# Kernel tuning notes

Measured on AMD Instinct MI355X. Metric: run time of the kernel, lower is better.

## Reference

```python
import jax, jax.numpy as jnp
import numpy as np
import math

NUM_SECTORS = 8
HIDDEN = 128
FEAT = 64
MAX_DIST = 10.0


def gru_last(x, Wih, Whh, bih, bhh):
    # PyTorch GRU (gate order r,z,n); x: (B,T,D) -> last hidden (B,H)
    B = x.shape[0]
    H = Whh.shape[1]
    xp = jnp.einsum('btd,gd->btg', x, Wih) + bih  # (B,T,3H)

    def step(h, xpt):
        hp = h @ Whh.T + bhh
        xr, xz, xn = jnp.split(xpt, 3, -1)
        hr, hz, hn = jnp.split(hp, 3, -1)
        r = jax.nn.sigmoid(xr + hr)
        z = jax.nn.sigmoid(xz + hz)
        n = jnp.tanh(xn + r * hn)
        h_new = (1.0 - z) * n + z * h
        return h_new, None

    h0 = jnp.zeros((B, H), x.dtype)
    hT, _ = jax.lax.scan(step, h0, jnp.swapaxes(xp, 0, 1))
    return hT


def setup_inputs() -> dict:
    key = jax.random.key(0)
    ks = iter(jax.random.split(key, 32))
    B, N, T = 2048, 64, 8
    H, Hn = HIDDEN, HIDDEN // 2
    s = 0.05

    def p(shape):
        return jax.random.normal(next(ks), shape, jnp.float32) * s

    inp = {
        'target_trajectory': jax.random.normal(next(ks), (B, T, 2), jnp.float32),
        'neighbor_trajectories': jax.random.normal(next(ks), (B, N, T, 2), jnp.float32),
        'relative_angles': jax.random.uniform(next(ks), (B, N), jnp.float32) * (2.0 * math.pi),
        'neighbor_mask': (jax.random.uniform(next(ks), (B, N)) > 0.2).astype(jnp.float32),
        # target GRU (H=128)
        'Wih_t': p((3 * H, 2)), 'Whh_t': p((3 * H, H)), 'bih_t': p((3 * H,)), 'bhh_t': p((3 * H,)),
        # neighbor GRU (H=64)
        'Wih_n': p((3 * Hn, 2)), 'Whh_n': p((3 * Hn, Hn)), 'bih_n': p((3 * Hn,)), 'bhh_n': p((3 * Hn,)),
        # sector encoder: 68 -> 128 -> 128
        'W1': p((H, 4 + Hn)), 'b1': p((H,)), 'W2': p((H, H)), 'b2': p((H,)),
        # fusion: 1152 -> 256 -> 128 -> 64
        'Wf1': p((2 * H, H + NUM_SECTORS * H)), 'bf1': p((2 * H,)),
        'Wf2': p((H, 2 * H)), 'bf2': p((H,)),
        'Wf3': p((FEAT, H)), 'bf3': p((FEAT,)),
        'ln_g': jnp.ones((FEAT,), jnp.float32), 'ln_b': jnp.zeros((FEAT,), jnp.float32),
    }
    return inp


def reference(target_trajectory, neighbor_trajectories, relative_angles, neighbor_mask,
              Wih_t, Whh_t, bih_t, bhh_t, Wih_n, Whh_n, bih_n, bhh_n,
              W1, b1, W2, b2, Wf1, bf1, Wf2, bf2, Wf3, bf3, ln_g, ln_b):
    B, N, T, D = neighbor_trajectories.shape
    S = NUM_SECTORS

    # trajectory encoders
    target_feature = gru_last(target_trajectory, Wih_t, Whh_t, bih_t, bhh_t)  # (B,128)
    nf = gru_last(neighbor_trajectories.reshape(B * N, T, D), Wih_n, Whh_n, bih_n, bhh_n)
    nf = nf.reshape(B, N, -1)  # (B,N,64)

    # geometry
    target_pos = target_trajectory[:, -1, :]                      # (B,2)
    npos = neighbor_trajectories[:, :, -1, :]                     # (B,N,2)
    dist = jnp.linalg.norm(npos - target_pos[:, None, :], axis=-1)  # (B,N)
    vel = neighbor_trajectories[:, :, -1, :] - neighbor_trajectories[:, :, -2, :]  # (B,N,2)

    # sector assignment (vectorized segment reduce over sectors)
    sector_size = 2.0 * math.pi / S
    sid = jnp.clip((relative_angles / sector_size).astype(jnp.int32), 0, S - 1)  # (B,N)
    valid = neighbor_mask > 0
    memb = ((sid[..., None] == jnp.arange(S)) & valid[..., None]).astype(dist.dtype)  # (B,N,S)

    count = memb.sum(1)                        # (B,S)
    nonempty = count > 0
    safe = jnp.maximum(count, 1.0)
    avg_d = jnp.where(nonempty, (dist[..., None] * memb).sum(1) / safe, 0.0)  # (B,S)
    avg_v = jnp.where(nonempty[..., None], jnp.einsum('bns,bnc->bsc', memb, vel) / safe[..., None], 0.0)

    w = jnp.exp(-dist / MAX_DIST)              # (B,N)
    wm = w[..., None] * memb                   # (B,N,S)
    wsum = wm.sum(1) + 1e-8                    # (B,S)
    wfeat = jnp.einsum('bns,bnh->bsh', wm, nf) / wsum[..., None]  # (B,S,64)

    sector_feats = jnp.concatenate([count[..., None], avg_d[..., None], avg_v, wfeat], axis=-1)  # (B,S,68)

    # sector encoder MLP (dropout off / eval)
    h = jax.nn.relu(sector_feats @ W1.T + b1)
    h = jax.nn.relu(h @ W2.T + b2)             # (B,S,128)
    enc = h.reshape(B, S * HIDDEN)

    combined = jnp.concatenate([target_feature, enc], axis=-1)  # (B,1152)
    f = jax.nn.relu(combined @ Wf1.T + bf1)
    f = jax.nn.relu(f @ Wf2.T + bf2)
    f = jax.nn.relu(f @ Wf3.T + bf3)           # (B,64)

    mu = f.mean(-1, keepdims=True)
    var = ((f - mu) ** 2).mean(-1, keepdims=True)
    return (f - mu) / jnp.sqrt(var + 1e-5) * ln_g + ln_b
```

## Files before the change

kernel.cpp:

```cpp
#include <hip/hip_runtime.h>

typedef __attribute__((ext_vector_type(8))) short short8;
typedef __attribute__((ext_vector_type(4))) float f32x4;

#define SGC (-1.44269504088896341f)
#define THC ( 2.88539008177792681f)

__device__ __forceinline__ unsigned short f2bf(float f){
  unsigned u = __float_as_uint(f);
  return (unsigned short)((u + 0x7fffu + ((u >> 16) & 1u)) >> 16);
}
__device__ __forceinline__ float bf2f(unsigned short b){
  return __uint_as_float(((unsigned)b) << 16);
}
__device__ __forceinline__ unsigned f2bf_cvt(float f){
  unsigned r;
  asm("v_cvt_pk_bf16_f32 %0, %1, %1" : "=v"(r) : "v"(f));
  return r;
}
__device__ __forceinline__ unsigned f2bf_pk(float lo, float hi){
  unsigned r;
  asm("v_cvt_pk_bf16_f32 %0, %1, %2" : "=v"(r) : "v"(lo), "v"(hi));
  return r;
}

__global__ __launch_bounds__(256) void k_prep(
    const float* __restrict__ Whh_t, const float* __restrict__ W1,
    const float* __restrict__ W2,    const float* __restrict__ Wf1,
    const float* __restrict__ Wf2,   const float* __restrict__ Wf3,
    const float* __restrict__ Whh_n,
    unsigned short* __restrict__ wgt)
{
  int i = blockIdx.x * 256 + threadIdx.x;
  if (i < 49152){
    int g = i >> 7;
    float s = (g < 256) ? SGC : THC;
    wgt[i] = f2bf(Whh_t[i] * s); return;
  }
  i -= 49152;
  if (i < 12288){ int r = i / 96, c = i % 96;
    wgt[49152 + i] = (c < 68) ? f2bf(W1[r*68 + c]) : (unsigned short)0; return; }
  i -= 12288;
  if (i < 16384){ wgt[61440 + i] = f2bf(W2[i]); return; }
  i -= 16384;
  if (i < 294912){ wgt[77824 + i] = f2bf(Wf1[i]); return; }
  i -= 294912;
  if (i < 32768){ wgt[372736 + i] = f2bf(Wf2[i]); return; }
  i -= 32768;
  if (i < 8192){ wgt[405504 + i] = f2bf(Wf3[i]); return; }
  i -= 8192;
  if (i < 12288){
    int g = i >> 6;
    float s = (g < 128) ? SGC : THC;
    wgt[413696 + i] = f2bf(Whh_n[i] * s); return;
  }
}

__global__ __launch_bounds__(256, 4) void k_gru_n(
    const float* __restrict__ ttraj, const float* __restrict__ ntraj,
    const float* __restrict__ rang,  const float* __restrict__ nmask,
    const float* __restrict__ Wih_n,
    const float* __restrict__ bih_n, const float* __restrict__ bhh_n,
    const unsigned short* __restrict__ wgt,
    const float* __restrict__ b1, const float* __restrict__ b2,
    unsigned short* __restrict__ combined)
{
  __shared__ char smem[38912];
  const int tid = threadIdx.x;
  const int w = tid >> 6, u = (tid >> 4) & 3, c = tid & 15;
  const int b = blockIdx.x;
  const unsigned short* whhN_b = wgt + 413696;

  unsigned short* whh2 = (unsigned short*)smem;
  unsigned short* wx   = whh2 + 12288;
  unsigned short* hall = (unsigned short*)(smem + 27648);
  unsigned short* hb   = hall + w * 1152;
  unsigned* xpk = (unsigned*)(smem + 36864);
  float* pool   = (float*)(smem + 36864);
  unsigned short* sfl = whh2;
  unsigned short* h1l = whh2 + 1536;

  for (int i = tid; i < 1536; i += 256){
    int nt = i >> 7, rem = i & 127;
    int hf = rem >> 6, uu = (rem >> 4) & 3, cc = rem & 15;
    *(short8*)&whh2[nt*1024 + hf*512 + (uu*16+cc)*8] =
        *(const short8*)&whhN_b[(nt*16+cc)*64 + hf*32 + uu*8];
  }
  if (tid < 192){
    int t = tid >> 4, cc = tid & 15;
    float s = (t < 8) ? SGC : THC;
    int g = (t < 4) ? (t*16 + cc) : (t < 8) ? (64 + (t-4)*16 + cc) : (128 + (t-8)*16 + cc);
    float bsum = (t < 8) ? (bih_n[g] + bhh_n[g]) : bih_n[g];
    unsigned short* p = &wx[t*128 + cc*8];
    *(short8*)p = (short8){0,0,0,0,0,0,0,0};
    p[0] = f2bf(Wih_n[g*2]   * s);
    p[1] = f2bf(Wih_n[g*2+1] * s);
    p[2] = f2bf(bsum * s);
  }
  {
    float4 v = ((const float4*)(ntraj + (size_t)b * 1024))[tid];
    int n = tid >> 2, p = (tid & 3) * 2;
    xpk[p*64 + n]       = f2bf_pk(v.x, v.y);
    xpk[(p+1)*64 + n]   = f2bf_pk(v.z, v.w);
  }
  __syncthreads();

  float bh_[4];
#pragma unroll
  for (int gt = 0; gt < 4; ++gt) bh_[gt] = bhh_n[128 + gt*16 + c] * THC;

  float hcur[4][4];
#pragma unroll
  for (int gt=0; gt<4; ++gt)
#pragma unroll
    for (int q=0; q<4; ++q) hcur[gt][q] = 0.0f;

  auto gates = [&](int gt, const f32x4& aR, const f32x4& aZ, const f32x4& aN, const f32x4& aX){
#pragma unroll
    for (int q = 0; q < 4; ++q){
      float r = __builtin_amdgcn_rcpf(1.0f + __builtin_amdgcn_exp2f(aR[q]));
      float z = __builtin_amdgcn_rcpf(1.0f + __builtin_amdgcn_exp2f(aZ[q]));
      float hn = aN[q] + bh_[gt];
      float pn = __builtin_fmaf(r, hn, aX[q]);
      float E = __builtin_amdgcn_exp2f(pn);
      float n = __builtin_fmaf(-2.0f, __builtin_amdgcn_rcpf(E + 1.0f), 1.0f);
      float hnew = __builtin_fmaf(z, hcur[gt][q] - n, n);
      hcur[gt][q] = hnew;
      hb[(u*4+q)*72 + gt*16 + c] = (unsigned short)f2bf_cvt(hnew);
    }
  };

  const int lane8 = (u*16 + c) * 8;
  const f32x4 zz = {0.f,0.f,0.f,0.f};

#pragma unroll 1
  for (int st = 0; st < 8; ++st){
    unsigned p01 = xpk[st*64 + w*16 + c];
    bool u0 = (u == 0);
    union { unsigned ui[4]; short8 s8; } a2u;
    a2u.ui[0] = u0 ? p01 : 0u;
    a2u.ui[1] = u0 ? 0x3F80u : 0u;
    a2u.ui[2] = 0u; a2u.ui[3] = 0u;
    short8 a2 = a2u.s8;

    if (st > 0){
      short8 a0 = *(short8*)&hb[c*72 + u*8];
      short8 a1 = *(short8*)&hb[c*72 + 32 + u*8];
#pragma unroll
      for (int gt = 0; gt < 4; ++gt){
        const unsigned short* pr = whh2 + gt*1024 + lane8;
        const unsigned short* pz = whh2 + (4+gt)*1024 + lane8;
        const unsigned short* pq = whh2 + (8+gt)*1024 + lane8;
        short8 bxr = *(const short8*)&wx[gt*128 + c*8];
        short8 bxz = *(const short8*)&wx[(4+gt)*128 + c*8];
        short8 bxn = *(const short8*)&wx[(8+gt)*128 + c*8];
        f32x4 aR = __builtin_amdgcn_mfma_f32_16x16x32_bf16(a0, *(const short8*)pr, zz, 0,0,0);
        aR = __builtin_amdgcn_mfma_f32_16x16x32_bf16(a1, *(const short8*)(pr+512), aR, 0,0,0);
        aR = __builtin_amdgcn_mfma_f32_16x16x32_bf16(a2, bxr, aR, 0,0,0);
        f32x4 aZ = __builtin_amdgcn_mfma_f32_16x16x32_bf16(a0, *(const short8*)pz, zz, 0,0,0);
        aZ = __builtin_amdgcn_mfma_f32_16x16x32_bf16(a1, *(const short8*)(pz+512), aZ, 0,0,0);
        aZ = __builtin_amdgcn_mfma_f32_16x16x32_bf16(a2, bxz, aZ, 0,0,0);
        f32x4 aN = __builtin_amdgcn_mfma_f32_16x16x32_bf16(a0, *(const short8*)pq, zz, 0,0,0);
        aN = __builtin_amdgcn_mfma_f32_16x16x32_bf16(a1, *(const short8*)(pq+512), aN, 0,0,0);
        f32x4 aX = __builtin_amdgcn_mfma_f32_16x16x32_bf16(a2, bxn, zz, 0,0,0);
        gates(gt, aR, aZ, aN, aX);
      }
    } else {
#pragma unroll
      for (int gt = 0; gt < 4; ++gt){
        short8 bxr = *(const short8*)&wx[gt*128 + c*8];
        short8 bxz = *(const short8*)&wx[(4+gt)*128 + c*8];
        short8 bxn = *(const short8*)&wx[(8+gt)*128 + c*8];
        f32x4 aR = __builtin_amdgcn_mfma_f32_16x16x32_bf16(a2, bxr, zz, 0,0,0);
        f32x4 aZ = __builtin_amdgcn_mfma_f32_16x16x32_bf16(a2, bxz, zz, 0,0,0);
        f32x4 aX = __builtin_amdgcn_mfma_f32_16x16x32_bf16(a2, bxn, zz, 0,0,0);
        gates(gt, aR, aZ, zz, aX);
      }
    }
  }
  __syncthreads();

  for (int i = tid; i < 1536; i += 256) sfl[i] = 0;
  if (tid < 64){
    int n = tid;
    const float* nb = ntraj + (size_t)b*1024 + n*16;
    float px = nb[14], py = nb[15];
    float vx = px - nb[12], vy = py - nb[13];
    float m   = nmask[(size_t)b*64 + n];
    float ang = rang[(size_t)b*64 + n];
    float tx = ttraj[(size_t)b*16 + 14], ty = ttraj[(size_t)b*16 + 15];
    float dx = px - tx, dy = py - ty;
    float dist = __builtin_amdgcn_sqrtf(dx*dx + dy*dy);
    int sid = (int)(ang / 0.78539816339744830962f);
    sid = sid < 0 ? 0 : (sid > 7 ? 7 : sid);
    bool valid = m > 0.0f;
    float wv = valid ? __builtin_amdgcn_exp2f(dist * -0.14426950408889634f) : 0.0f;
    pool[n]       = valid ? dist : 0.0f;
    pool[64 + n]  = valid ? vx   : 0.0f;
    pool[128 + n] = valid ? vy   : 0.0f;
    pool[192 + n] = wv;
    pool[256 + n] = valid ? (float)sid : -1.0f;
  }
  __syncthreads();
  if (tid < 8){
    int s = tid;
    float cnt=0.f, sd=0.f, sx=0.f, sy=0.f, sw=0.f;
#pragma unroll 4
    for (int n=0; n<64; ++n){
      if (pool[256+n] == (float)s){
        cnt += 1.f; sd += pool[n]; sx += pool[64+n]; sy += pool[128+n]; sw += pool[192+n];
      }
    }
    float inv = (cnt > 0.f) ? __builtin_amdgcn_rcpf(cnt) : 0.f;
    pool[320 + s] = cnt;
    pool[328 + s] = sd * inv;
    pool[336 + s] = sx * inv;
    pool[344 + s] = sy * inv;
    pool[352 + s] = __builtin_amdgcn_rcpf(sw + 1e-8f);
  }
  __syncthreads();
#pragma unroll
  for (int rep = 0; rep < 2; ++rep){
    int p = tid + rep*256;
    int s = p >> 6, h = p & 63;
    float fs = (float)s;
    float a = 0.f;
#pragma unroll 4
    for (int n = 0; n < 64; ++n){
      float wmv = (pool[256+n] == fs) ? pool[192+n] : 0.f;
      float nf  = bf2f(hall[(n>>4)*1152 + (n&15)*72 + h]);
      a += wmv * nf;
    }
    sfl[s*96 + 4 + h] = (unsigned short)f2bf_cvt(a * pool[352+s]);
  }
  if (tid < 32){
    int s = tid >> 2, cc = tid & 3;
    sfl[s*96 + cc] = (unsigned short)f2bf_cvt(pool[320 + cc*8 + s]);
  }
  __syncthreads();

  const unsigned short* w1b = wgt + 49152;
  const unsigned short* w2b = wgt + 61440;
  f32x4 accA[2];
#pragma unroll
  for (int i=0;i<2;++i) accA[i] = zz;
#pragma unroll
  for (int kc=0; kc<3; ++kc){
    short8 a = (short8){0,0,0,0,0,0,0,0};
    if (c < 8) a = *(const short8*)&sfl[c*96 + kc*32 + u*8];
#pragma unroll
    for (int i=0;i<2;++i){
      int nt = w*2 + i;
      short8 bb = *(const short8*)&w1b[(nt*16+c)*96 + kc*32 + u*8];
      accA[i] = __builtin_amdgcn_mfma_f32_16x16x32_bf16(a, bb, accA[i], 0,0,0);
    }
  }
#pragma unroll
  for (int i=0;i<2;++i){
    int nt = w*2 + i;
    float bias = b1[nt*16 + c];
#pragma unroll
    for (int q=0;q<4;++q){
      float v = accA[i][q] + bias; v = v > 0.f ? v : 0.f;
      h1l[(u*4+q)*136 + nt*16 + c] = (unsigned short)f2bf_cvt(v);
    }
  }
  __syncthreads();

  f32x4 accB[2];
#pragma unroll
  for (int i=0;i<2;++i) accB[i] = zz;
#pragma unroll
  for (int kc=0; kc<4; ++kc){
    short8 a = *(short8*)&h1l[c*136 + kc*32 + u*8];
#pragma unroll
    for (int i=0;i<2;++i){
      int nt = w*2 + i;
      short8 bb = *(const short8*)&w2b[(nt*16+c)*128 + kc*32 + u*8];
      accB[i] = __builtin_amdgcn_mfma_f32_16x16x32_bf16(a, bb, accB[i], 0,0,0);
    }
  }
#pragma unroll
  for (int i=0;i<2;++i){
    int nt = w*2 + i;
    float bias = b2[nt*16 + c];
#pragma unroll
    for (int q=0;q<4;++q){
      int row = u*4 + q;
      if (row < 8){
        float v = accB[i][q] + bias; v = v > 0.f ? v : 0.f;
        combined[(size_t)b*1152 + 128 + row*128 + nt*16 + c] = (unsigned short)f2bf_cvt(v);
      }
    }
  }
}

__global__ __launch_bounds__(256) void k_gru_t(
    const float* __restrict__ ttraj,
    const float* __restrict__ Wih_t, const float* __restrict__ bih_t, const float* __restrict__ bhh_t,
    const unsigned short* __restrict__ wgt,
    unsigned short* __restrict__ combined)
{
  __shared__ char smem[9728];
  const int tid = threadIdx.x, w = tid >> 6, u = (tid >> 4) & 3, c = tid & 15;
  unsigned short* hb0 = (unsigned short*)smem;
  unsigned short* hb1 = (unsigned short*)(smem + 4352);
  float* xs = (float*)(smem + 8704);

  xs[tid] = ttraj[(size_t)blockIdx.x*256 + tid];

  int ntg[6];
  ntg[0] = 2*w; ntg[1] = 2*w+1;
  ntg[2] = 8+2*w; ntg[3] = 9+2*w;
  ntg[4] = 16+2*w; ntg[5] = 17+2*w;

  short8 Bf[6][4];
#pragma unroll
  for (int lt2 = 0; lt2 < 6; ++lt2){
    const unsigned short* wp = wgt + (ntg[lt2]*16 + c)*128 + u*8;
#pragma unroll
    for (int kk = 0; kk < 4; ++kk)
      Bf[lt2][kk] = *(const short8*)(wp + kk*32);
  }

  float Wr0[2],Wr1[2],BR[2],Wz0[2],Wz1[2],BZ[2],Wn0[2],Wn1[2],BI[2],BH[2];
#pragma unroll
  for (int gt = 0; gt < 2; ++gt){
    int g = w*32 + gt*16 + c;
    Wr0[gt]=Wih_t[g*2]*SGC;        Wr1[gt]=Wih_t[g*2+1]*SGC;        BR[gt]=(bih_t[g]+bhh_t[g])*SGC;
    Wz0[gt]=Wih_t[(128+g)*2]*SGC;  Wz1[gt]=Wih_t[(128+g)*2+1]*SGC;  BZ[gt]=(bih_t[128+g]+bhh_t[128+g])*SGC;
    Wn0[gt]=Wih_t[(256+g)*2]*THC;  Wn1[gt]=Wih_t[(256+g)*2+1]*THC;  BI[gt]=bih_t[256+g]*THC; BH[gt]=bhh_t[256+g]*THC;
  }
  float hcur[2][4];
#pragma unroll
  for (int gt=0; gt<2; ++gt)
#pragma unroll
    for (int q=0; q<4; ++q) hcur[gt][q] = 0.0f;
  __syncthreads();

#pragma unroll 1
  for (int st = 0; st < 8; ++st){
    unsigned short* rbuf = (st & 1) ? hb0 : hb1;
    unsigned short* wbuf = (st & 1) ? hb1 : hb0;
    f32x4 acc[6];
    if (st > 0){
      short8 a0 = *(short8*)&rbuf[c*136 + u*8];
      short8 a1 = *(short8*)&rbuf[c*136 + 32 + u*8];
      short8 a2 = *(short8*)&rbuf[c*136 + 64 + u*8];
      short8 a3 = *(short8*)&rbuf[c*136 + 96 + u*8];
#pragma unroll
      for (int lt2 = 0; lt2 < 6; ++lt2){
        f32x4 t = {0.f,0.f,0.f,0.f};
        t = __builtin_amdgcn_mfma_f32_16x16x32_bf16(a0, Bf[lt2][0], t, 0,0,0);
        t = __builtin_amdgcn_mfma_f32_16x16x32_bf16(a1, Bf[lt2][1], t, 0,0,0);
        t = __builtin_amdgcn_mfma_f32_16x16x32_bf16(a2, Bf[lt2][2], t, 0,0,0);
        acc[lt2] = __builtin_amdgcn_mfma_f32_16x16x32_bf16(a3, Bf[lt2][3], t, 0,0,0);
      }
    } else {
#pragma unroll
      for (int lt2 = 0; lt2 < 6; ++lt2) acc[lt2] = (f32x4){0.f,0.f,0.f,0.f};
    }
#pragma unroll
    for (int gt = 0; gt < 2; ++gt){
#pragma unroll
      for (int q = 0; q < 4; ++q){
        int sq = u*4 + q;
        float x0 = xs[sq*16 + st*2], x1 = xs[sq*16 + st*2 + 1];
        float rp = __builtin_fmaf(Wr0[gt], x0, __builtin_fmaf(Wr1[gt], x1, acc[gt][q] + BR[gt]));
        float zp = __builtin_fmaf(Wz0[gt], x0, __builtin_fmaf(Wz1[gt], x1, acc[2+gt][q] + BZ[gt]));
        float r = __builtin_amdgcn_rcpf(1.0f + __builtin_amdgcn_exp2f(rp));
        float z = __builtin_amdgcn_rcpf(1.0f + __builtin_amdgcn_exp2f(zp));
        float hnv = acc[4+gt][q] + BH[gt];
        float pn = __builtin_fmaf(Wn0[gt], x0, __builtin_fmaf(Wn1[gt], x1, __builtin_fmaf(r, hnv, BI[gt])));
        float E = __builtin_amdgcn_exp2f(pn);
        float n = __builtin_fmaf(-2.0f, __builtin_amdgcn_rcpf(E + 1.0f), 1.0f);
        float hnew = __builtin_fmaf(z, hcur[gt][q] - n, n);
        hcur[gt][q] = hnew;
        if (st < 7){
          wbuf[sq*136 + w*32 + gt*16 + c] = (unsigned short)f2bf_cvt(hnew);
        } else {
          int row = blockIdx.x*16 + sq;
          combined[(size_t)row*1152 + w*32 + gt*16 + c] = (unsigned short)f2bf_cvt(hnew);
        }
      }
    }
    if (st < 7) __syncthreads();
  }
}

__global__ __launch_bounds__(256) void k_head(
    const unsigned short* __restrict__ combined,
    const unsigned short* __restrict__ wgt,
    const float* __restrict__ bf1, const float* __restrict__ bf2, const float* __restrict__ bf3,
    const float* __restrict__ lng, const float* __restrict__ lnb,
    float* __restrict__ out)
{
  __shared__ char smem[15104];
  const int tid = threadIdx.x, w = tid >> 6, u = (tid >> 4) & 3, c = tid & 15;
  unsigned short* f1b = (unsigned short*)smem;
  unsigned short* f2b = (unsigned short*)(smem + 8448);
  float* bf1s = (float*)(smem + 12800); float* bf2s = (float*)(smem + 13824);
  float* bf3s = (float*)(smem + 14336);
  float* lngs = (float*)(smem + 14592); float* lnbs = (float*)(smem + 14848);
  const unsigned short* wf1b = wgt + 77824;
  const unsigned short* wf2b = wgt + 372736;
  const unsigned short* wf3b = wgt + 405504;
  bf1s[tid] = bf1[tid];
  if (tid < 128) bf2s[tid] = bf2[tid];
  if (tid < 64){ bf3s[tid] = bf3[tid]; lngs[tid] = lng[tid]; lnbs[tid] = lnb[tid]; }
  __syncthreads();
  const int rowb = blockIdx.x * 16;

  f32x4 acc[4];
#pragma unroll
  for (int i=0; i<4; ++i) acc[i] = (f32x4){0.f,0.f,0.f,0.f};
#pragma unroll 4
  for (int kc=0; kc<36; ++kc){
    short8 a = *(const short8*)&combined[(size_t)(rowb + c)*1152 + kc*32 + u*8];
#pragma unroll
    for (int i=0; i<4; ++i){
      int nt = w*4 + i;
      short8 bb = *(const short8*)&wf1b[(size_t)(nt*16+c)*1152 + kc*32 + u*8];
      acc[i] = __builtin_amdgcn_mfma_f32_16x16x32_bf16(a, bb, acc[i], 0,0,0);
    }
  }
#pragma unroll
  for (int i=0; i<4; ++i){
    int nt = w*4 + i;
    float bias = bf1s[nt*16+c];
#pragma unroll
    for (int q=0; q<4; ++q){
      float v = acc[i][q] + bias; v = v > 0.f ? v : 0.f;
      f1b[(u*4+q)*264 + nt*16 + c] = (unsigned short)f2bf_cvt(v);
    }
  }
  __syncthreads();

  f32x4 acc2[2];
#pragma unroll
  for (int i=0; i<2; ++i) acc2[i] = (f32x4){0.f,0.f,0.f,0.f};
#pragma unroll
  for (int kc=0; kc<8; ++kc){
    short8 a = *(short8*)&f1b[c*264 + kc*32 + u*8];
#pragma unroll
    for (int i=0; i<2; ++i){
      int nt = w*2 + i;
      short8 bb = *(const short8*)&wf2b[(nt*16+c)*256 + kc*32 + u*8];
      acc2[i] = __builtin_amdgcn_mfma_f32_16x16x32_bf16(a, bb, acc2[i], 0,0,0);
    }
  }
#pragma unroll
  for (int i=0; i<2; ++i){
    int nt = w*2 + i;
    float bias = bf2s[nt*16+c];
#pragma unroll
    for (int q=0; q<4; ++q){
      float v = acc2[i][q] + bias; v = v > 0.f ? v : 0.f;
      f2b[(u*4+q)*136 + nt*16 + c] = (unsigned short)f2bf_cvt(v);
    }
  }
  __syncthreads();

  f32x4 acc3[4];
#pragma unroll
  for (int nt=0; nt<4; ++nt) acc3[nt] = (f32x4){0.f,0.f,0.f,0.f};
#pragma unroll
  for (int kc=0; kc<4; ++kc){
    short8 a = *(short8*)&f2b[c*136 + kc*32 + u*8];
#pragma unroll
    for (int nt=0; nt<4; ++nt){
      short8 bb = *(const short8*)&wf3b[(nt*16+c)*128 + kc*32 + u*8];
      acc3[nt] = __builtin_amdgcn_mfma_f32_16x16x32_bf16(a, bb, acc3[nt], 0,0,0);
    }
  }
  if (w == 0){
    float v[4][4];
#pragma unroll
    for (int nt=0; nt<4; ++nt){
      float bias = bf3s[nt*16+c];
#pragma unroll
      for (int q=0; q<4; ++q){
        float t = acc3[nt][q] + bias; v[nt][q] = t > 0.f ? t : 0.f;
      }
    }
#pragma unroll
    for (int q=0; q<4; ++q){
      float p = v[0][q] + v[1][q] + v[2][q] + v[3][q];
      p += __shfl_xor(p, 1); p += __shfl_xor(p, 2); p += __shfl_xor(p, 4); p += __shfl_xor(p, 8);
      float mu = p * 0.015625f;
      float d0 = v[0][q]-mu, d1 = v[1][q]-mu, d2 = v[2][q]-mu, d3 = v[3][q]-mu;
      float p2 = d0*d0 + d1*d1 + d2*d2 + d3*d3;
      p2 += __shfl_xor(p2, 1); p2 += __shfl_xor(p2, 2); p2 += __shfl_xor(p2, 4); p2 += __shfl_xor(p2, 8);
      float rstd = __builtin_amdgcn_rsqf(p2 * 0.015625f + 1e-5f);
      int row = rowb + u*4 + q;
#pragma unroll
      for (int nt=0; nt<4; ++nt){
        int col = nt*16 + c;
        out[(size_t)row*64 + col] = (v[nt][q] - mu) * rstd * lngs[col] + lnbs[col];
      }
    }
  }
}

extern "C" void kernel_launch(void* const* d_in, const int* in_sizes, int n_in,
                              void* d_out, int out_size, void* d_ws, size_t ws_size,
                              hipStream_t stream)
{
  const float* ttraj = (const float*)d_in[0];
  const float* ntraj = (const float*)d_in[1];
  const float* rang  = (const float*)d_in[2];
  const float* nmask = (const float*)d_in[3];
  const float* Wih_t = (const float*)d_in[4];
  const float* Whh_t = (const float*)d_in[5];
  const float* bih_t = (const float*)d_in[6];
  const float* bhh_t = (const float*)d_in[7];
  const float* Wih_n = (const float*)d_in[8];
  const float* Whh_n = (const float*)d_in[9];
  const float* bih_n = (const float*)d_in[10];
  const float* bhh_n = (const float*)d_in[11];
  const float* W1  = (const float*)d_in[12];
  const float* b1  = (const float*)d_in[13];
  const float* W2  = (const float*)d_in[14];
  const float* b2  = (const float*)d_in[15];
  const float* Wf1 = (const float*)d_in[16];
  const float* bf1 = (const float*)d_in[17];
  const float* Wf2 = (const float*)d_in[18];
  const float* bf2 = (const float*)d_in[19];
  const float* Wf3 = (const float*)d_in[20];
  const float* bf3 = (const float*)d_in[21];
  const float* lng = (const float*)d_in[22];
  const float* lnb = (const float*)d_in[23];

  char* ws = (char*)d_ws;
  unsigned short* combined = (unsigned short*)ws;
  unsigned short* wgt      = (unsigned short*)(ws + 8388608);

  hipLaunchKernelGGL(k_prep, dim3(1664), dim3(256), 0, stream,
                     Whh_t, W1, W2, Wf1, Wf2, Wf3, Whh_n, wgt);
  hipLaunchKernelGGL(k_gru_n, dim3(2048), dim3(256), 0, stream,
                     ttraj, ntraj, rang, nmask, Wih_n, bih_n, bhh_n, wgt, b1, b2, combined);
  hipLaunchKernelGGL(k_gru_t, dim3(128), dim3(256), 0, stream,
                     ttraj, Wih_t, bih_t, bhh_t, wgt, combined);
  hipLaunchKernelGGL(k_head, dim3(128), dim3(256), 0, stream,
                     combined, wgt, bf1, bf2, bf3, lng, lnb, (float*)d_out);
}
```

Before: 139.8 us.

## Pack four batch items per 1024-thread block in neighbor GRU kernel

The neighbor GRU kernel now handles four batch elements per workgroup of 1024 threads instead of one per 256-thread block. The recurrent weight matrix and input-projection tiles are staged into LDS once and shared by all four sub-blocks, while each sub-block gets its own hidden-state, trajectory and pooling scratch. The aim is to cut the repeated global-to-LDS weight staging and raise the number of resident waves per CU. In exchange every barrier now spans 16 waves, and the stricter launch bounds may force register spills.

Measured after the change: 140.9 us. About the same (+0.8%).

```diff
diff --git a/kernel.cpp b/kernel.cpp
--- a/kernel.cpp
+++ b/kernel.cpp
@@ -56,7 +56,7 @@
   }
 }
 
-__global__ __launch_bounds__(256, 4) void k_gru_n(
+__global__ __launch_bounds__(1024, 8) void k_gru_n(
     const float* __restrict__ ttraj, const float* __restrict__ ntraj,
     const float* __restrict__ rang,  const float* __restrict__ nmask,
     const float* __restrict__ Wih_n,
@@ -65,22 +65,24 @@
     const float* __restrict__ b1, const float* __restrict__ b2,
     unsigned short* __restrict__ combined)
 {
-  __shared__ char smem[38912];
+  __shared__ char smem[72704];
   const int tid = threadIdx.x;
-  const int w = tid >> 6, u = (tid >> 4) & 3, c = tid & 15;
-  const int b = blockIdx.x;
+  const int bi = tid >> 8, lt = tid & 255;
+  const int w = lt >> 6, u = (lt >> 4) & 3, c = lt & 15;
+  const int b = blockIdx.x * 4 + bi;
   const unsigned short* whhN_b = wgt + 413696;
 
   unsigned short* whh2 = (unsigned short*)smem;
   unsigned short* wx   = whh2 + 12288;
-  unsigned short* hall = (unsigned short*)(smem + 27648);
+  char* pb = smem + 27648 + bi * 11264;
+  unsigned short* hall = (unsigned short*)pb;
   unsigned short* hb   = hall + w * 1152;
-  unsigned* xpk = (unsigned*)(smem + 36864);
-  float* pool   = (float*)(smem + 36864);
-  unsigned short* sfl = whh2;
-  unsigned short* h1l = whh2 + 1536;
-
-  for (int i = tid; i < 1536; i += 256){
+  unsigned* xpk = (unsigned*)(pb + 9216);
+  float* pool   = (float*)(pb + 9216);
+  unsigned short* sfl = whh2 + bi * 1536;
+  unsigned short* h1l = hall;
+
+  for (int i = tid; i < 1536; i += 1024){
     int nt = i >> 7, rem = i & 127;
     int hf = rem >> 6, uu = (rem >> 4) & 3, cc = rem & 15;
     *(short8*)&whh2[nt*1024 + hf*512 + (uu*16+cc)*8] =
@@ -98,8 +100,8 @@
     p[2] = f2bf(bsum * s);
   }
   {
-    float4 v = ((const float4*)(ntraj + (size_t)b * 1024))[tid];
-    int n = tid >> 2, p = (tid & 3) * 2;
+    float4 v = ((const float4*)(ntraj + (size_t)b * 1024))[lt];
+    int n = lt >> 2, p = (lt & 3) * 2;
     xpk[p*64 + n]       = f2bf_pk(v.x, v.y);
     xpk[(p+1)*64 + n]   = f2bf_pk(v.z, v.w);
   }
@@ -180,9 +182,9 @@
   }
   __syncthreads();
 
-  for (int i = tid; i < 1536; i += 256) sfl[i] = 0;
-  if (tid < 64){
-    int n = tid;
+  for (int i = lt; i < 1536; i += 256) sfl[i] = 0;
+  if (lt < 64){
+    int n = lt;
     const float* nb = ntraj + (size_t)b*1024 + n*16;
     float px = nb[14], py = nb[15];
     float vx = px - nb[12], vy = py - nb[13];
@@ -202,8 +204,8 @@
     pool[256 + n] = valid ? (float)sid : -1.0f;
   }
   __syncthreads();
-  if (tid < 8){
-    int s = tid;
+  if (lt < 8){
+    int s = lt;
     float cnt=0.f, sd=0.f, sx=0.f, sy=0.f, sw=0.f;
 #pragma unroll 4
     for (int n=0; n<64; ++n){
@@ -221,7 +223,7 @@
   __syncthreads();
 #pragma unroll
   for (int rep = 0; rep < 2; ++rep){
-    int p = tid + rep*256;
+    int p = lt + rep*256;
     int s = p >> 6, h = p & 63;
     float fs = (float)s;
     float a = 0.f;
@@ -233,8 +235,8 @@
     }
     sfl[s*96 + 4 + h] = (unsigned short)f2bf_cvt(a * pool[352+s]);
   }
-  if (tid < 32){
-    int s = tid >> 2, cc = tid & 3;
+  if (lt < 32){
+    int s = lt >> 2, cc = lt & 3;
     sfl[s*96 + cc] = (unsigned short)f2bf_cvt(pool[320 + cc*8 + s]);
   }
   __syncthreads();
@@ -537,7 +539,7 @@
 
   hipLaunchKernelGGL(k_prep, dim3(1664), dim3(256), 0, stream,
                      Whh_t, W1, W2, Wf1, Wf2, Wf3, Whh_n, wgt);
-  hipLaunchKernelGGL(k_gru_n, dim3(2048), dim3(256), 0, stream,
+  hipLaunchKernelGGL(k_gru_n, dim3(512), dim3(1024), 0, stream,
                      ttraj, ntraj, rang, nmask, Wih_n, bih_n, bhh_n, wgt, b1, b2, combined);
   hipLaunchKernelGGL(k_gru_t, dim3(128), dim3(256), 0, stream,
                      ttraj, Wih_t, bih_t, bhh_t, wgt, combined);
```
